# Optimization experiments

Hardware: AMD Instinct MI355X
Metric: run time of the kernel (lower is better)

## Reference

```python
import jax, jax.numpy as jnp
import numpy as np

EPS = 1e-8


def setup_inputs() -> dict:
    key = jax.random.key(0)
    k1, k2, k3, k4, k5 = jax.random.split(key, 5)
    B, D, N, M = 16, 128, 2048, 2048
    return {
        "src_embedding": jax.random.normal(k1, (B, D, N), dtype=jnp.float32),
        "tgt_embedding": jax.random.normal(k2, (B, D, M), dtype=jnp.float32),
        "src": jax.random.normal(k3, (B, 3, N), dtype=jnp.float32),
        "tgt": jax.random.normal(k4, (B, 3, M), dtype=jnp.float32),
        "temperature": jax.random.uniform(k5, (B, 1), dtype=jnp.float32),
    }


def reference(src_embedding, tgt_embedding, src, tgt, temperature):
    B = src.shape[0]
    # cross-attention scores [B, N, M] and row softmax
    scores = jax.nn.softmax(
        jnp.einsum("bdn,bdm->bnm", src_embedding, tgt_embedding), axis=-1
    )
    # hard correspondence: argmax over tgt points, gather tgt coords -> [B, 3, N]
    idx = jnp.argmax(scores, axis=-1)                      # [B, N]
    src_corr = jnp.take_along_axis(tgt, idx[:, None, :].repeat(3, axis=1), axis=-1)
    # entropy-based weights (note: original applies -1/(entropy+eps), kept faithfully)
    w = jnp.sum(scores * jnp.log(scores + EPS), axis=-1)   # [B, N]
    w = -1.0 / (w + EPS)
    w_norm = w / (jnp.sum(w, axis=-1, keepdims=True) + EPS)  # [B, N]
    wn = w_norm[:, None, :]                                # [B, 1, N]
    src_centroid = jnp.sum(src * wn, axis=2, keepdims=True)       # [B, 3, 1]
    tgt_centroid = jnp.sum(src_corr * wn, axis=2, keepdims=True)  # [B, 3, 1]
    src_centered = src - src_centroid
    corr_centered = (src_corr - tgt_centroid) * wn
    # 3x3 cross-covariance per batch
    H = jnp.einsum("bin,bjn->bij", src_centered, corr_centered) + jnp.eye(3, dtype=src.dtype) * EPS
    # batched 3x3 SVD entirely on device; torch.svd returns V s.t. H = U S V^T
    U, S, Vh = jnp.linalg.svd(H)
    V = jnp.swapaxes(Vh, -1, -2)
    r = jnp.einsum("bij,bkj->bik", V, U)                   # V @ U^T
    det = jnp.linalg.det(r)                                # [B]
    diag = jnp.tile(jnp.eye(3, dtype=src.dtype), (B, 1, 1)).at[:, 2, 2].set(det)
    R = jnp.einsum("bij,bjk,blk->bil", V, diag, U)         # V @ diag @ U^T
    t = (jnp.einsum("bij,bjk->bik", -R, src_centroid) + tgt_centroid).reshape(B, 3)
    return R, t, scores
```

## Files before the change

### kernel.cpp

```cpp
#include <hip/hip_runtime.h>
#include <math.h>

constexpr int B = 16, D = 128, N = 2048, M = 2048;
#define EPSF 1e-8f

__global__ __launch_bounds__(256) void gemm_logits(
    const float* __restrict__ Ae, const float* __restrict__ Be,
    float* __restrict__ out)
{
    const int b  = blockIdx.z;
    const int n0 = blockIdx.y * 128;
    const int m0 = blockIdx.x * 128;
    const float* A  = Ae + (size_t)b * D * N;
    const float* Bm = Be + (size_t)b * D * M;
    float* C = out + (size_t)b * N * M;

    __shared__ float As[8][128];
    __shared__ float Bs[8][128];

    const int t  = threadIdx.x;
    const int lr = t >> 5;
    const int lc = (t & 31) * 4;
    const int tx = t & 15;
    const int ty = t >> 4;

    float acc[8][8];
#pragma unroll
    for (int i = 0; i < 8; ++i)
#pragma unroll
        for (int j = 0; j < 8; ++j) acc[i][j] = 0.f;

    for (int d0 = 0; d0 < D; d0 += 8) {
        const float4 av = *(const float4*)(A  + (size_t)(d0 + lr) * N + n0 + lc);
        const float4 bv = *(const float4*)(Bm + (size_t)(d0 + lr) * M + m0 + lc);
        *(float4*)(&As[lr][lc]) = av;
        *(float4*)(&Bs[lr][lc]) = bv;
        __syncthreads();
#pragma unroll
        for (int kk = 0; kk < 8; ++kk) {
            float a[8], bb[8];
            *(float4*)(&a[0])  = *(const float4*)(&As[kk][ty * 8]);
            *(float4*)(&a[4])  = *(const float4*)(&As[kk][ty * 8 + 4]);
            *(float4*)(&bb[0]) = *(const float4*)(&Bs[kk][tx * 8]);
            *(float4*)(&bb[4]) = *(const float4*)(&Bs[kk][tx * 8 + 4]);
#pragma unroll
            for (int i = 0; i < 8; ++i)
#pragma unroll
                for (int j = 0; j < 8; ++j)
                    acc[i][j] = fmaf(a[i], bb[j], acc[i][j]);
        }
        __syncthreads();
    }

#pragma unroll
    for (int i = 0; i < 8; ++i) {
        float4 c0 = make_float4(acc[i][0], acc[i][1], acc[i][2], acc[i][3]);
        float4 c1 = make_float4(acc[i][4], acc[i][5], acc[i][6], acc[i][7]);
        size_t off = (size_t)(n0 + ty * 8 + i) * M + (m0 + tx * 8);
        *(float4*)(C + off)     = c0;
        *(float4*)(C + off + 4) = c1;
    }
}

__global__ __launch_bounds__(256) void softmax_rows(
    float* __restrict__ scores, float* __restrict__ wout, int* __restrict__ idxout)
{
    const int row = blockIdx.x;
    float* p = scores + (size_t)row * M;
    const int t = threadIdx.x;

    float4 v0 = ((const float4*)p)[t];
    float4 v1 = ((const float4*)p)[t + 256];
    float vals[8] = {v0.x, v0.y, v0.z, v0.w, v1.x, v1.y, v1.z, v1.w};
    int   idxs[8] = {t*4, t*4+1, t*4+2, t*4+3,
                     1024 + t*4, 1024 + t*4 + 1, 1024 + t*4 + 2, 1024 + t*4 + 3};

    float m = vals[0]; int mi = idxs[0];
#pragma unroll
    for (int k = 1; k < 8; ++k)
        if (vals[k] > m) { m = vals[k]; mi = idxs[k]; }

    __shared__ float sv[256];
    __shared__ int   si[256];
    sv[t] = m; si[t] = mi;
    __syncthreads();
    for (int s = 128; s > 0; s >>= 1) {
        if (t < s) {
            float ov = sv[t + s]; int oi = si[t + s];
            if (ov > sv[t] || (ov == sv[t] && oi < si[t])) { sv[t] = ov; si[t] = oi; }
        }
        __syncthreads();
    }
    const float rowmax = sv[0];
    const int   rowidx = si[0];
    __syncthreads();

    float e[8]; float lsum = 0.f;
#pragma unroll
    for (int k = 0; k < 8; ++k) { e[k] = expf(vals[k] - rowmax); lsum += e[k]; }
    sv[t] = lsum;
    __syncthreads();
    for (int s = 128; s > 0; s >>= 1) { if (t < s) sv[t] += sv[t + s]; __syncthreads(); }
    const float inv = 1.0f / sv[0];
    __syncthreads();

    float ent = 0.f;
#pragma unroll
    for (int k = 0; k < 8; ++k) {
        float pk = e[k] * inv;
        e[k] = pk;
        ent += pk * logf(pk + EPSF);
    }
    ((float4*)p)[t]       = make_float4(e[0], e[1], e[2], e[3]);
    ((float4*)p)[t + 256] = make_float4(e[4], e[5], e[6], e[7]);

    sv[t] = ent;
    __syncthreads();
    for (int s = 128; s > 0; s >>= 1) { if (t < s) sv[t] += sv[t + s]; __syncthreads(); }
    if (t == 0) {
        wout[row]   = -1.0f / (sv[0] + EPSF);
        idxout[row] = rowidx;
    }
}

__device__ inline float block_sum_256(float v, float* red, int t)
{
    red[t] = v; __syncthreads();
    for (int s = 128; s > 0; s >>= 1) { if (t < s) red[t] += red[t + s]; __syncthreads(); }
    float r = red[0]; __syncthreads();
    return r;
}

__global__ __launch_bounds__(256) void kabsch(
    const float* __restrict__ src, const float* __restrict__ tgt,
    const float* __restrict__ wraw, const int* __restrict__ idxv,
    float* __restrict__ Rout, float* __restrict__ tout)
{
    const int b = blockIdx.x;
    const int t = threadIdx.x;
    const float* S  = src  + (size_t)b * 3 * N;
    const float* T  = tgt  + (size_t)b * 3 * M;
    const float* w  = wraw + (size_t)b * N;
    const int*  idx = idxv + (size_t)b * N;

    __shared__ float red[256];

    float w8[8]; int i8[8];
    float s8[8][3], g8[8][3];
    float lsum = 0.f;
#pragma unroll
    for (int k = 0; k < 8; ++k) {
        int n = t + 256 * k;
        w8[k] = w[n];
        i8[k] = idx[n];
        lsum += w8[k];
#pragma unroll
        for (int i = 0; i < 3; ++i) {
            s8[k][i] = S[i * N + n];
            g8[k][i] = T[i * M + i8[k]];
        }
    }
    const float W = block_sum_256(lsum, red, t) + EPSF;

    float c[6] = {0, 0, 0, 0, 0, 0};
#pragma unroll
    for (int k = 0; k < 8; ++k) {
        float wn = w8[k] / W;
#pragma unroll
        for (int i = 0; i < 3; ++i) {
            c[i]     += wn * s8[k][i];
            c[3 + i] += wn * g8[k][i];
        }
    }
    float cen[6];
    for (int i = 0; i < 6; ++i) cen[i] = block_sum_256(c[i], red, t);

    float h[9] = {0};
#pragma unroll
    for (int k = 0; k < 8; ++k) {
        float wn = w8[k] / W;
        float a0 = s8[k][0] - cen[0], a1 = s8[k][1] - cen[1], a2 = s8[k][2] - cen[2];
        float b0 = (g8[k][0] - cen[3]) * wn;
        float b1 = (g8[k][1] - cen[4]) * wn;
        float b2 = (g8[k][2] - cen[5]) * wn;
        h[0] += a0 * b0; h[1] += a0 * b1; h[2] += a0 * b2;
        h[3] += a1 * b0; h[4] += a1 * b1; h[5] += a1 * b2;
        h[6] += a2 * b0; h[7] += a2 * b1; h[8] += a2 * b2;
    }
    float hr[9];
    for (int i = 0; i < 9; ++i) hr[i] = block_sum_256(h[i], red, t);

    if (t == 0) {
        double H[3][3];
        for (int i = 0; i < 3; ++i)
            for (int j = 0; j < 3; ++j)
                H[i][j] = (double)hr[i * 3 + j] + (i == j ? 1e-8 : 0.0);

        double A[3][3];
        for (int i = 0; i < 3; ++i)
            for (int j = 0; j < 3; ++j)
                A[i][j] = H[0][i] * H[0][j] + H[1][i] * H[1][j] + H[2][i] * H[2][j];

        double V[3][3] = {{1, 0, 0}, {0, 1, 0}, {0, 0, 1}};
        const int PP[3] = {0, 0, 1}, QQ[3] = {1, 2, 2};
        for (int sweep = 0; sweep < 30; ++sweep) {
            for (int r = 0; r < 3; ++r) {
                int p = PP[r], q = QQ[r];
                double apq = A[p][q];
                if (fabs(apq) < 1e-300) continue;
                double theta = (A[q][q] - A[p][p]) / (2.0 * apq);
                double tt = (theta >= 0 ? 1.0 : -1.0) /
                            (fabs(theta) + sqrt(theta * theta + 1.0));
                double cc = 1.0 / sqrt(tt * tt + 1.0);
                double ss = tt * cc;
                for (int k = 0; k < 3; ++k) {
                    double akp = A[k][p], akq = A[k][q];
                    A[k][p] = cc * akp - ss * akq;
                    A[k][q] = ss * akp + cc * akq;
                }
                for (int k = 0; k < 3; ++k) {
                    double apk = A[p][k], aqk = A[q][k];
                    A[p][k] = cc * apk - ss * aqk;
                    A[q][k] = ss * apk + cc * aqk;
                }
                for (int k = 0; k < 3; ++k) {
                    double vkp = V[k][p], vkq = V[k][q];
                    V[k][p] = cc * vkp - ss * vkq;
                    V[k][q] = ss * vkp + cc * vkq;
                }
            }
        }
        double ev[3] = {A[0][0], A[1][1], A[2][2]};
        int ord[3] = {0, 1, 2};
        for (int i = 0; i < 2; ++i)
            for (int j = i + 1; j < 3; ++j)
                if (ev[ord[j]] > ev[ord[i]]) { int tmp = ord[i]; ord[i] = ord[j]; ord[j] = tmp; }
        double Vs[3][3];
        for (int i = 0; i < 3; ++i)
            for (int j = 0; j < 3; ++j)
                Vs[i][j] = V[i][ord[j]];

        double U[3][3];
        for (int j = 0; j < 2; ++j) {
            double u0 = H[0][0] * Vs[0][j] + H[0][1] * Vs[1][j] + H[0][2] * Vs[2][j];
            double u1 = H[1][0] * Vs[0][j] + H[1][1] * Vs[1][j] + H[1][2] * Vs[2][j];
            double u2 = H[2][0] * Vs[0][j] + H[2][1] * Vs[1][j] + H[2][2] * Vs[2][j];
            if (j == 1) {
                double d0 = u0 * U[0][0] + u1 * U[1][0] + u2 * U[2][0];
                u0 -= d0 * U[0][0]; u1 -= d0 * U[1][0]; u2 -= d0 * U[2][0];
            }
            double nn = sqrt(u0 * u0 + u1 * u1 + u2 * u2);
            if (nn < 1e-150) {
                u0 = (j == 0) ? 1.0 : -U[1][0];
                u1 = (j == 0) ? 0.0 : U[0][0];
                u2 = 0.0;
                nn = sqrt(u0 * u0 + u1 * u1 + u2 * u2);
                if (nn < 1e-150) { u0 = 0; u1 = 0; u2 = 1; nn = 1; }
            }
            U[0][j] = u0 / nn; U[1][j] = u1 / nn; U[2][j] = u2 / nn;
        }
        U[0][2] = U[1][0] * U[2][1] - U[2][0] * U[1][1];
        U[1][2] = U[2][0] * U[0][1] - U[0][0] * U[2][1];
        U[2][2] = U[0][0] * U[1][1] - U[1][0] * U[0][1];

        double r[3][3];
        for (int i = 0; i < 3; ++i)
            for (int j = 0; j < 3; ++j)
                r[i][j] = Vs[i][0] * U[j][0] + Vs[i][1] * U[j][1] + Vs[i][2] * U[j][2];
        double det = r[0][0] * (r[1][1] * r[2][2] - r[1][2] * r[2][1])
                   - r[0][1] * (r[1][0] * r[2][2] - r[1][2] * r[2][0])
                   + r[0][2] * (r[1][0] * r[2][1] - r[1][1] * r[2][0]);

        double R[3][3];
        for (int i = 0; i < 3; ++i)
            for (int j = 0; j < 3; ++j)
                R[i][j] = Vs[i][0] * U[j][0] + Vs[i][1] * U[j][1] + det * Vs[i][2] * U[j][2];

        double tv[3];
        for (int i = 0; i < 3; ++i)
            tv[i] = (double)cen[3 + i]
                  - (R[i][0] * cen[0] + R[i][1] * cen[1] + R[i][2] * cen[2]);

        for (int i = 0; i < 3; ++i)
            for (int j = 0; j < 3; ++j)
                Rout[b * 9 + i * 3 + j] = (float)R[i][j];
        for (int i = 0; i < 3; ++i)
            tout[b * 3 + i] = (float)tv[i];
    }
}

extern "C" void kernel_launch(void* const* d_in, const int* in_sizes, int n_in,
                              void* d_out, int out_size, void* d_ws, size_t ws_size,
                              hipStream_t stream)
{
    const float* src_emb = (const float*)d_in[0];
    const float* tgt_emb = (const float*)d_in[1];
    const float* src     = (const float*)d_in[2];
    const float* tgt     = (const float*)d_in[3];

    float* out    = (float*)d_out;
    float* Rout   = out;
    float* tout   = out + B * 9;
    float* scores = out + B * 12;

    float* wws   = (float*)d_ws;
    int*   idxws = (int*)((float*)d_ws + B * N);

    dim3 g1(M / 128, N / 128, B);
    gemm_logits<<<g1, 256, 0, stream>>>(src_emb, tgt_emb, scores);
    softmax_rows<<<B * N, 256, 0, stream>>>(scores, wws, idxws);
    kabsch<<<B, 256, 0, stream>>>(src, tgt, wws, idxws, Rout, tout);
}
```

Baseline: 575.2 us.

## Fuse row argmax into GEMM epilogue via atomicMax and shuffle-reduce softmax

The GEMM epilogue packs each logit with its column into a sortable 64-bit key, reduces across lanes with shuffles, and issues an atomicMax per row, so the softmax kernel no longer needs its own max/argmax reduction. The softmax sum and entropy reductions switch from shared-memory tree loops to wavefront shuffles plus a four-entry combine. The B tile columns are remapped to a split 4+4 layout, which changes LDS access and makes the C stores contiguous across lanes. A workspace-zeroing kernel and per-row 64-bit atomics add some cost, and ties resolve to the lowest index through the packed key.

```diff
diff --git a/kernel.cpp b/kernel.cpp
--- a/kernel.cpp
+++ b/kernel.cpp
@@ -4,9 +4,28 @@
 constexpr int B = 16, D = 128, N = 2048, M = 2048;
 #define EPSF 1e-8f
 
+__device__ __forceinline__ unsigned int sortable_u32(float f) {
+    unsigned int u = __float_as_uint(f);
+    return (u & 0x80000000u) ? ~u : (u | 0x80000000u);
+}
+__device__ __forceinline__ float unsortable_f32(unsigned int s) {
+    unsigned int u = (s & 0x80000000u) ? (s & 0x7FFFFFFFu) : ~s;
+    return __uint_as_float(u);
+}
+__device__ __forceinline__ unsigned long long shfl_xor_u64(unsigned long long v, int mask) {
+    unsigned int hi = (unsigned int)(v >> 32), lo = (unsigned int)v;
+    hi = __shfl_xor(hi, mask); lo = __shfl_xor(lo, mask);
+    return ((unsigned long long)hi << 32) | lo;
+}
+
+__global__ void init_ws(unsigned long long* __restrict__ amax) {
+    int i = blockIdx.x * 256 + threadIdx.x;
+    if (i < B * N) amax[i] = 0ull;
+}
+
 __global__ __launch_bounds__(256) void gemm_logits(
     const float* __restrict__ Ae, const float* __restrict__ Be,
-    float* __restrict__ out)
+    float* __restrict__ out, unsigned long long* __restrict__ amax)
 {
     const int b  = blockIdx.z;
     const int n0 = blockIdx.y * 128;
@@ -41,8 +60,8 @@
             float a[8], bb[8];
             *(float4*)(&a[0])  = *(const float4*)(&As[kk][ty * 8]);
             *(float4*)(&a[4])  = *(const float4*)(&As[kk][ty * 8 + 4]);
-            *(float4*)(&bb[0]) = *(const float4*)(&Bs[kk][tx * 8]);
-            *(float4*)(&bb[4]) = *(const float4*)(&Bs[kk][tx * 8 + 4]);
+            *(float4*)(&bb[0]) = *(const float4*)(&Bs[kk][tx * 4]);
+            *(float4*)(&bb[4]) = *(const float4*)(&Bs[kk][64 + tx * 4]);
 #pragma unroll
             for (int i = 0; i < 8; ++i)
 #pragma unroll
@@ -54,55 +73,60 @@
 
 #pragma unroll
     for (int i = 0; i < 8; ++i) {
-        float4 c0 = make_float4(acc[i][0], acc[i][1], acc[i][2], acc[i][3]);
-        float4 c1 = make_float4(acc[i][4], acc[i][5], acc[i][6], acc[i][7]);
-        size_t off = (size_t)(n0 + ty * 8 + i) * M + (m0 + tx * 8);
-        *(float4*)(C + off)     = c0;
-        *(float4*)(C + off + 4) = c1;
+        const int row = n0 + ty * 8 + i;
+        const int gr  = b * N + row;
+        unsigned long long pk = 0ull;
+#pragma unroll
+        for (int j = 0; j < 8; ++j) {
+            const int col = m0 + ((j < 4) ? tx * 4 + j : 64 + tx * 4 + (j - 4));
+            unsigned long long key =
+                ((unsigned long long)sortable_u32(acc[i][j]) << 32) |
+                (unsigned int)(M - 1 - col);
+            pk = pk > key ? pk : key;
+        }
+        size_t off = (size_t)row * M + m0;
+        *(float4*)(C + off + tx * 4)      = make_float4(acc[i][0], acc[i][1], acc[i][2], acc[i][3]);
+        *(float4*)(C + off + 64 + tx * 4) = make_float4(acc[i][4], acc[i][5], acc[i][6], acc[i][7]);
+
+#pragma unroll
+        for (int msk = 8; msk > 0; msk >>= 1) {
+            unsigned long long o = shfl_xor_u64(pk, msk);
+            pk = pk > o ? pk : o;
+        }
+        if (tx == 0) atomicMax(&amax[gr], pk);
     }
 }
 
 __global__ __launch_bounds__(256) void softmax_rows(
-    float* __restrict__ scores, float* __restrict__ wout, int* __restrict__ idxout)
+    float* __restrict__ scores, const unsigned long long* __restrict__ amax,
+    float* __restrict__ wout, int* __restrict__ idxout)
 {
     const int row = blockIdx.x;
     float* p = scores + (size_t)row * M;
-    const int t = threadIdx.x;
+    const int t   = threadIdx.x;
+    const int wid = t >> 6;
+
+    __shared__ float redA[4], redB[4];
+
+    const unsigned long long key = amax[row];
+    const float rowmax = unsortable_f32((unsigned int)(key >> 32));
+    const int   rowidx = (M - 1) - (int)(key & 0xFFFFFFFFull);
 
     float4 v0 = ((const float4*)p)[t];
     float4 v1 = ((const float4*)p)[t + 256];
-    float vals[8] = {v0.x, v0.y, v0.z, v0.w, v1.x, v1.y, v1.z, v1.w};
-    int   idxs[8] = {t*4, t*4+1, t*4+2, t*4+3,
-                     1024 + t*4, 1024 + t*4 + 1, 1024 + t*4 + 2, 1024 + t*4 + 3};
-
-    float m = vals[0]; int mi = idxs[0];
-#pragma unroll
-    for (int k = 1; k < 8; ++k)
-        if (vals[k] > m) { m = vals[k]; mi = idxs[k]; }
-
-    __shared__ float sv[256];
-    __shared__ int   si[256];
-    sv[t] = m; si[t] = mi;
+    float e[8] = {expf(v0.x - rowmax), expf(v0.y - rowmax),
+                  expf(v0.z - rowmax), expf(v0.w - rowmax),
+                  expf(v1.x - rowmax), expf(v1.y - rowmax),
+                  expf(v1.z - rowmax), expf(v1.w - rowmax)};
+
+    float lsum = 0.f;
+#pragma unroll
+    for (int k = 0; k < 8; ++k) lsum += e[k];
+#pragma unroll
+    for (int m = 32; m > 0; m >>= 1) lsum += __shfl_xor(lsum, m);
+    if ((t & 63) == 0) redA[wid] = lsum;
     __syncthreads();
-    for (int s = 128; s > 0; s >>= 1) {
-        if (t < s) {
-            float ov = sv[t + s]; int oi = si[t + s];
-            if (ov > sv[t] || (ov == sv[t] && oi < si[t])) { sv[t] = ov; si[t] = oi; }
-        }
-        __syncthreads();
-    }
-    const float rowmax = sv[0];
-    const int   rowidx = si[0];
-    __syncthreads();
-
-    float e[8]; float lsum = 0.f;
-#pragma unroll
-    for (int k = 0; k < 8; ++k) { e[k] = expf(vals[k] - rowmax); lsum += e[k]; }
-    sv[t] = lsum;
-    __syncthreads();
-    for (int s = 128; s > 0; s >>= 1) { if (t < s) sv[t] += sv[t + s]; __syncthreads(); }
-    const float inv = 1.0f / sv[0];
-    __syncthreads();
+    const float inv = 1.0f / (redA[0] + redA[1] + redA[2] + redA[3]);
 
     float ent = 0.f;
 #pragma unroll
@@ -114,11 +138,12 @@
     ((float4*)p)[t]       = make_float4(e[0], e[1], e[2], e[3]);
     ((float4*)p)[t + 256] = make_float4(e[4], e[5], e[6], e[7]);
 
-    sv[t] = ent;
+#pragma unroll
+    for (int m = 32; m > 0; m >>= 1) ent += __shfl_xor(ent, m);
+    if ((t & 63) == 0) redB[wid] = ent;
     __syncthreads();
-    for (int s = 128; s > 0; s >>= 1) { if (t < s) sv[t] += sv[t + s]; __syncthreads(); }
     if (t == 0) {
-        wout[row]   = -1.0f / (sv[0] + EPSF);
+        wout[row]   = -1.0f / ((redB[0] + redB[1] + redB[2] + redB[3]) + EPSF);
         idxout[row] = rowidx;
     }
 }
@@ -303,11 +328,13 @@
     float* tout   = out + B * 9;
     float* scores = out + B * 12;
 
-    float* wws   = (float*)d_ws;
-    int*   idxws = (int*)((float*)d_ws + B * N);
-
+    unsigned long long* amax  = (unsigned long long*)d_ws;
+    float*              wws   = (float*)(amax + B * N);
+    int*                idxws = (int*)(wws + B * N);
+
+    init_ws<<<(B * N + 255) / 256, 256, 0, stream>>>(amax);
     dim3 g1(M / 128, N / 128, B);
-    gemm_logits<<<g1, 256, 0, stream>>>(src_emb, tgt_emb, scores);
-    softmax_rows<<<B * N, 256, 0, stream>>>(scores, wws, idxws);
+    gemm_logits<<<g1, 256, 0, stream>>>(src_emb, tgt_emb, scores, amax);
+    softmax_rows<<<B * N, 256, 0, stream>>>(scores, amax, wws, idxws);
     kabsch<<<B, 256, 0, stream>>>(src, tgt, wws, idxws, Rout, tout);
 }
```

New measurement: 584.9 us. Within noise of the previous version (+1.7%).
